# Performance work log

Hardware: AMD Instinct MI355X
Metric: run time of the kernel (lower is better)

The kernel has to match this reference:

```python
import jax, jax.numpy as jnp
import numpy as np

B, S, D, H = 4, 2048, 1024, 16
HD = D // H  # 64


def setup_inputs() -> dict:
    key = jax.random.key(0)
    ks = jax.random.split(key, 16)
    inv = 1.0 / np.sqrt(D)
    inv_hd = 1.0 / np.sqrt(D)
    inp = {
        "query": jax.random.normal(ks[0], (B, S, D), jnp.float32),
        "key": jax.random.normal(ks[1], (B, S, D), jnp.float32),
        "value": jax.random.normal(ks[2], (B, S, D), jnp.float32),
        # causal mask: True entries are masked out (masked_fill semantics)
        "mask": jnp.triu(jnp.ones((S, S), jnp.bool_), k=1),
        # weights stored [in, out] (math identical to torch x @ W.T)
        "Wq": jax.random.normal(ks[3], (D, D), jnp.float32) * inv,
        "Wk": jax.random.normal(ks[4], (D, D), jnp.float32) * inv,
        "Wv": jax.random.normal(ks[5], (D, D), jnp.float32) * inv,
        "wq_h": jax.random.normal(ks[6], (D, HD), jnp.float32) * inv_hd,
        "bq_h": jax.random.normal(ks[7], (HD,), jnp.float32) * inv_hd,
        "wk_h": jax.random.normal(ks[8], (D, HD), jnp.float32) * inv_hd,
        "bk_h": jax.random.normal(ks[9], (HD,), jnp.float32) * inv_hd,
        "wv_h": jax.random.normal(ks[10], (D, HD), jnp.float32) * inv_hd,
        "bv_h": jax.random.normal(ks[11], (HD,), jnp.float32) * inv_hd,
        "Wo": jax.random.normal(ks[12], (D, D), jnp.float32) * inv,
    }
    return inp


def reference(query, key, value, mask, Wq, Wk, Wv, wq_h, bq_h, wk_h, bk_h, wv_h, bv_h, Wo):
    # full-width projections
    q = jnp.einsum('bsd,de->bse', query, Wq)
    k = jnp.einsum('bsd,de->bse', key, Wk)
    v = jnp.einsum('bsd,de->bse', value, Wv)
    # per-head projections: the torch loop reuses the SAME weights every
    # iteration, so all H head outputs are identical -> compute once.
    qh = jnp.einsum('bsd,dh->bsh', q, wq_h) + bq_h  # [B,S,HD]
    kh = jnp.einsum('bsd,dh->bsh', k, wk_h) + bk_h
    vh = jnp.einsum('bsd,dh->bsh', v, wv_h) + bv_h
    scores = jnp.einsum('bsh,bth->bst', qh, kh) / jnp.sqrt(jnp.float32(HD))
    scores = jnp.where(mask, jnp.float32(-1e9), scores)
    attn = jax.nn.softmax(scores, axis=-1)
    out_h = jnp.einsum('bst,bth->bsh', attn, vh)  # [B,S,HD]
    out = jnp.tile(out_h, (1, 1, H))  # cat of H identical heads -> [B,S,D]
    # final linear; dropout is identity at inference
    return jnp.einsum('bsd,de->bse', out, Wo)
```

## Files before the change

### kernel.cpp

```cpp
#include <hip/hip_runtime.h>
#include <math.h>

#define S_LEN 2048
#define BATCH 4
#define DMODEL 1024
#define HDIM 64
#define NROWS (BATCH * S_LEN)

typedef __attribute__((ext_vector_type(8))) short bf16x8;
typedef __attribute__((ext_vector_type(4))) float f32x4;

__device__ inline ushort f2bf(float f) {
    union { float f; uint u; } v{f};
    uint r = v.u + 0x7fffu + ((v.u >> 16) & 1u);
    return (ushort)(r >> 16);
}

__device__ inline bf16x8 cvt8(float4 a, float4 b) {
    bf16x8 r;
    r[0] = (short)f2bf(a.x); r[1] = (short)f2bf(a.y);
    r[2] = (short)f2bf(a.z); r[3] = (short)f2bf(a.w);
    r[4] = (short)f2bf(b.x); r[5] = (short)f2bf(b.y);
    r[6] = (short)f2bf(b.z); r[7] = (short)f2bf(b.w);
    return r;
}

__global__ __launch_bounds__(256) void transpose_wh(
    const float* __restrict__ B0, const float* __restrict__ B1, const float* __restrict__ B2,
    ushort* __restrict__ T0, ushort* __restrict__ T1, ushort* __restrict__ T2)
{
    const int z = blockIdx.y;
    const float* B = (z == 0) ? B0 : (z == 1) ? B1 : B2;
    ushort* T      = (z == 0) ? T0 : (z == 1) ? T1 : T2;
    const int kr0 = blockIdx.x * 64;
    __shared__ ushort Ts[64][72];
    const int t = threadIdx.x;

    #pragma unroll
    for (int q = 0; q < 4; ++q) {
        int u   = t * 4 + q;
        int row = u >> 4;
        int c4  = (u & 15) << 2;
        float4 v = *reinterpret_cast<const float4*>(
            B + (size_t)(kr0 + row) * 64 + c4);
        Ts[row][c4 + 0] = f2bf(v.x); Ts[row][c4 + 1] = f2bf(v.y);
        Ts[row][c4 + 2] = f2bf(v.z); Ts[row][c4 + 3] = f2bf(v.w);
    }
    __syncthreads();
    #pragma unroll
    for (int q = 0; q < 2; ++q) {
        int u  = t * 2 + q;
        int h  = u >> 3;
        int k8 = (u & 7) << 3;
        uint4 o;
        uint* ow = reinterpret_cast<uint*>(&o);
        #pragma unroll
        for (int i = 0; i < 4; ++i)
            ow[i] = (uint)Ts[k8 + 2 * i][h] | ((uint)Ts[k8 + 2 * i + 1][h] << 16);
        *reinterpret_cast<uint4*>(T + (size_t)h * 1024 + kr0 + k8) = o;
    }
}

__global__ __launch_bounds__(256) void prep_direct(
    const float* __restrict__ A0, const float* __restrict__ A1, const float* __restrict__ A2,
    const ushort* __restrict__ W0, const ushort* __restrict__ W1, const ushort* __restrict__ W2,
    ushort* __restrict__ T0, ushort* __restrict__ T1, ushort* __restrict__ T2)
{
    const int z = blockIdx.y;
    const float* A  = (z == 0) ? A0 : (z == 1) ? A1 : A2;
    const ushort* W = (z == 0) ? W0 : (z == 1) ? W1 : W2;
    ushort* T       = (z == 0) ? T0 : (z == 1) ? T1 : T2;

    __shared__ float Pr[4][16][64];

    const int t    = threadIdx.x;
    const int w    = t >> 6;
    const int lane = t & 63;
    const int lg   = lane >> 4;
    const int lc   = lane & 15;
    const int r0   = blockIdx.x * 16;

    const float*  Ap = A + (size_t)(r0 + lc) * 1024 + (w << 8) + (lg << 3);
    const ushort* Bp = W + (size_t)lc * 1024 + (w << 8) + (lg << 3);

    f32x4 acc[4] = {};
    float4 a0[2], a1[2];
    uint4  bl[2][4];

    #pragma unroll
    for (int d = 0; d < 2; ++d) {
        a0[d] = *reinterpret_cast<const float4*>(Ap + d * 32);
        a1[d] = *reinterpret_cast<const float4*>(Ap + d * 32 + 4);
        #pragma unroll
        for (int n = 0; n < 4; ++n)
            bl[d][n] = *reinterpret_cast<const uint4*>(Bp + n * 16384 + d * 32);
    }

    #pragma unroll
    for (int ks = 0; ks < 8; ++ks) {
        const int d = ks & 1;
        bf16x8 af = cvt8(a0[d], a1[d]);
        bf16x8 bfr[4];
        #pragma unroll
        for (int n = 0; n < 4; ++n)
            bfr[n] = __builtin_bit_cast(bf16x8, bl[d][n]);
        if (ks < 6) {
            a0[d] = *reinterpret_cast<const float4*>(Ap + (ks + 2) * 32);
            a1[d] = *reinterpret_cast<const float4*>(Ap + (ks + 2) * 32 + 4);
            #pragma unroll
            for (int n = 0; n < 4; ++n)
                bl[d][n] = *reinterpret_cast<const uint4*>(Bp + n * 16384 + (ks + 2) * 32);
        }
        #pragma unroll
        for (int n = 0; n < 4; ++n)
            acc[n] = __builtin_amdgcn_mfma_f32_16x16x32_bf16(af, bfr[n], acc[n], 0, 0, 0);
    }

    #pragma unroll
    for (int n = 0; n < 4; ++n)
        #pragma unroll
        for (int reg = 0; reg < 4; ++reg)
            Pr[w][4 * lg + reg][16 * n + lc] = acc[n][reg];
    __syncthreads();

    const int row = t >> 4;
    const int col = (t & 15) << 2;
    float s[4];
    #pragma unroll
    for (int i = 0; i < 4; ++i)
        s[i] = Pr[0][row][col + i] + Pr[1][row][col + i] +
               Pr[2][row][col + i] + Pr[3][row][col + i];
    #pragma unroll
    for (int i = 0; i < 4; ++i)
        T[(size_t)(col + i) * 1024 + r0 + row] = f2bf(s[i]);
}

__global__ __launch_bounds__(64) void proj_sw(
    const float* __restrict__ A0, const float* __restrict__ A1, const float* __restrict__ A2,
    const ushort* __restrict__ W0, const ushort* __restrict__ W1, const ushort* __restrict__ W2,
    const float* __restrict__ b0, const float* __restrict__ b1, const float* __restrict__ b2,
    ushort* __restrict__ O0, ushort* __restrict__ O1, ushort* __restrict__ O2)
{
    const int z = blockIdx.y;
    const float* A    = (z == 0) ? A0 : (z == 1) ? A1 : A2;
    const ushort* W   = (z == 0) ? W0 : (z == 1) ? W1 : W2;
    const float* bias = (z == 0) ? b0 : (z == 1) ? b1 : b2;
    ushort* O         = (z == 0) ? O0 : (z == 1) ? O1 : O2;

    __shared__ __align__(16) ushort Abuf[2][16][64];

    const int l  = threadIdx.x;
    const int lg = l >> 4;
    const int lc = l & 15;
    const int wu = lc >> 1;
    const int wh = lc & 1;
    const int r0 = blockIdx.x * 16;

    f32x4 acc[4] = {};

#define LOADA(R, c)                                                           \
    _Pragma("unroll")                                                         \
    for (int j = 0; j < 4; ++j)                                               \
        R[j] = *reinterpret_cast<const float4*>(                              \
            A + (size_t)(r0 + 4 * j + lg) * 1024 + (c) * 64 + lc * 4);

#define PROCESS(c, R, BUF)                                                    \
    {                                                                         \
        bf16x8 bfr[4][2];                                                     \
        _Pragma("unroll")                                                     \
        for (int a = 0; a < 4; ++a)                                           \
            _Pragma("unroll")                                                 \
            for (int s = 0; s < 2; ++s)                                       \
                bfr[a][s] = *reinterpret_cast<const bf16x8*>(                 \
                    W + (size_t)(16 * a + lc) * 1024 + (c) * 64 + s * 32 +    \
                    lg * 8);                                                  \
        _Pragma("unroll")                                                     \
        for (int j = 0; j < 4; ++j) {                                         \
            uint2 pk;                                                         \
            pk.x = (uint)f2bf(R[j].x) | ((uint)f2bf(R[j].y) << 16);           \
            pk.y = (uint)f2bf(R[j].z) | ((uint)f2bf(R[j].w) << 16);           \
            int row = 4 * j + lg;                                             \
            char* dst = (char*)Abuf + (BUF) * 2048 + row * 128 +              \
                        ((wu ^ (row & 7)) << 4) + wh * 8;                     \
            *reinterpret_cast<uint2*>(dst) = pk;                              \
        }                                                                     \
        _Pragma("unroll")                                                     \
        for (int s = 0; s < 2; ++s) {                                         \
            const char* src = (const char*)Abuf + (BUF) * 2048 + lc * 128 +   \
                              (((s * 4 + lg) ^ (lc & 7)) << 4);               \
            bf16x8 af = *reinterpret_cast<const bf16x8*>(src);                \
            _Pragma("unroll")                                                 \
            for (int a = 0; a < 4; ++a)                                       \
                acc[a] = __builtin_amdgcn_mfma_f32_16x16x32_bf16(             \
                    af, bfr[a][s], acc[a], 0, 0, 0);                          \
        }                                                                     \
    }

    float4 ra[4], rb[4];
    LOADA(ra, 0)
    #pragma unroll
    for (int cc = 0; cc < 8; ++cc) {
        LOADA(rb, 2 * cc + 1)
        PROCESS(2 * cc, ra, 0)
        if (cc < 7) LOADA(ra, 2 * cc + 2)
        PROCESS(2 * cc + 1, rb, 1)
    }
#undef LOADA
#undef PROCESS

    #pragma unroll
    for (int a = 0; a < 4; ++a) {
        float bv = bias[16 * a + lc];
        #pragma unroll
        for (int reg = 0; reg < 4; ++reg)
            O[(size_t)(r0 + 4 * lg + reg) * 64 + 16 * a + lc] =
                f2bf(acc[a][reg] + bv);
    }
}

__global__ __launch_bounds__(256) void fold_wo(const float* __restrict__ Wo,
                                               ushort* __restrict__ WoT)
{
    int idx = blockIdx.x * 256 + threadIdx.x;
    int j = idx >> 10;
    int e = idx & 1023;
    float s = 0.f;
    #pragma unroll
    for (int h = 0; h < 16; ++h)
        s += Wo[(size_t)((h << 6) + j) * 1024 + e];
    WoT[(size_t)e * 64 + j] = f2bf(s);
}

__global__ __launch_bounds__(256) void transpose_v(const ushort* __restrict__ vh,
                                                   ushort* __restrict__ vhT)
{
    const int b  = blockIdx.y;
    const int r0 = blockIdx.x * 64;
    __shared__ ushort T[64][72];
    const int t = threadIdx.x;

    #pragma unroll
    for (int q = 0; q < 2; ++q) {
        int u  = t * 2 + q;
        int s  = u >> 3;
        int d8 = (u & 7) << 3;
        uint4 v = *reinterpret_cast<const uint4*>(
            vh + ((size_t)b * S_LEN + r0 + s) * 64 + d8);
        *reinterpret_cast<uint4*>(&T[s][d8]) = v;
    }
    __syncthreads();
    #pragma unroll
    for (int q = 0; q < 2; ++q) {
        int u  = t * 2 + q;
        int d  = u >> 3;
        int s8 = (u & 7) << 3;
        uint4 o;
        uint* ow = reinterpret_cast<uint*>(&o);
        #pragma unroll
        for (int i = 0; i < 4; ++i)
            ow[i] = (uint)T[s8 + 2 * i][d] | ((uint)T[s8 + 2 * i + 1][d] << 16);
        *reinterpret_cast<uint4*>(
            vhT + (size_t)b * 64 * S_LEN + (size_t)d * S_LEN + r0 + s8) = o;
    }
}

__global__ __launch_bounds__(256) void flash_mfma(
    const ushort* __restrict__ qh, const ushort* __restrict__ kh,
    const ushort* __restrict__ vhT,
    float* __restrict__ Opart, float* __restrict__ mpart, float* __restrict__ lpart)
{
    const int b = blockIdx.y;
    const int u = blockIdx.x;
    int gi = 0;
    #pragma unroll
    for (int gg = 0; gg < 7; ++gg)
        if (u >= 2 * (gg + 1) * (gg + 2)) gi = gg + 1;
    const int rem = u - 2 * gi * (gi + 1);
    const int dq  = rem / (gi + 1);
    const int c   = rem - dq * (gi + 1);
    const int qt  = 4 * gi + dq;
    const int r0  = qt * 64;
    const int kvbase = c << 8;
    const int slot = b * 144 + u;

    __shared__ ushort Qs[64][72];
    __shared__ ushort Ks[64][72];
    __shared__ ushort Vt[64][72];
    __shared__ ushort Pw[4][16][72];

    const int t    = threadIdx.x;
    const int w    = t >> 6;
    const int lane = t & 63;
    const int lg   = lane >> 4;
    const int lc   = lane & 15;

    const ushort* qb  = qh  + (size_t)b * S_LEN * 64;
    const ushort* kb  = kh  + (size_t)b * S_LEN * 64;
    const ushort* vtb = vhT + (size_t)b * 64 * S_LEN;

    #pragma unroll
    for (int q = 0; q < 2; ++q) {
        int uu  = t * 2 + q;
        int row = uu >> 3;
        int c8  = (uu & 7) << 3;
        *reinterpret_cast<uint4*>(&Qs[row][c8]) =
            *reinterpret_cast<const uint4*>(qb + (size_t)(r0 + row) * 64 + c8);
    }
    __syncthreads();
    bf16x8 qf0 = *reinterpret_cast<const bf16x8*>(&Qs[16 * w + lc][lg * 8]);
    bf16x8 qf1 = *reinterpret_cast<const bf16x8*>(&Qs[16 * w + lc][32 + lg * 8]);

    f32x4 od[4] = {};
    float m = -INFINITY, lsum = 0.f;
    const int qrow = r0 + 16 * w + lc;

    const int ntt = min(4, ((r0 + 63 - kvbase) >> 6) + 1);
    for (int tt = 0; tt < ntt; ++tt) {
        const int t0 = kvbase + (tt << 6);
        __syncthreads();
        #pragma unroll
        for (int q = 0; q < 2; ++q) {
            int uu  = t * 2 + q;
            int row = uu >> 3;
            int c8  = (uu & 7) << 3;
            *reinterpret_cast<uint4*>(&Ks[row][c8]) =
                *reinterpret_cast<const uint4*>(kb + (size_t)(t0 + row) * 64 + c8);
            *reinterpret_cast<uint4*>(&Vt[row][c8]) =
                *reinterpret_cast<const uint4*>(vtb + (size_t)row * S_LEN + t0 + c8);
        }
        __syncthreads();

        if (t0 <= r0 + 16 * w + 15) {
            f32x4 s[4] = {};
            #pragma unroll
            for (int a = 0; a < 4; ++a) {
                bf16x8 kf0 = *reinterpret_cast<const bf16x8*>(&Ks[16 * a + lc][lg * 8]);
                bf16x8 kf1 = *reinterpret_cast<const bf16x8*>(&Ks[16 * a + lc][32 + lg * 8]);
                s[a] = __builtin_amdgcn_mfma_f32_16x16x32_bf16(kf0, qf0, s[a], 0, 0, 0);
                s[a] = __builtin_amdgcn_mfma_f32_16x16x32_bf16(kf1, qf1, s[a], 0, 0, 0);
            }
            float rm = -1e30f;
            #pragma unroll
            for (int a = 0; a < 4; ++a)
                #pragma unroll
                for (int reg = 0; reg < 4; ++reg) {
                    int kv = t0 + 16 * a + 4 * lg + reg;
                    float v = s[a][reg] * 0.125f;
                    if (kv > qrow) v = -1e30f;
                    s[a][reg] = v;
                    rm = fmaxf(rm, v);
                }
            rm = fmaxf(rm, __shfl_xor(rm, 16));
            rm = fmaxf(rm, __shfl_xor(rm, 32));
            float mn = fmaxf(m, rm);
            float sc = __expf(m - mn);
            float rs = 0.f;
            #pragma unroll
            for (int a = 0; a < 4; ++a)
                #pragma unroll
                for (int reg = 0; reg < 4; ++reg) {
                    float p = __expf(s[a][reg] - mn);
                    s[a][reg] = p;
                    rs += p;
                }
            rs += __shfl_xor(rs, 16);
            rs += __shfl_xor(rs, 32);
            lsum = lsum * sc + rs;
            m = mn;
            #pragma unroll
            for (int di = 0; di < 4; ++di) od[di] *= sc;

            #pragma unroll
            for (int a = 0; a < 4; ++a)
                #pragma unroll
                for (int rp = 0; rp < 2; ++rp) {
                    uint pk = (uint)f2bf(s[a][2 * rp]) |
                              ((uint)f2bf(s[a][2 * rp + 1]) << 16);
                    *reinterpret_cast<uint*>(&Pw[w][lc][16 * a + 4 * lg + 2 * rp]) = pk;
                }
            bf16x8 pf0 = *reinterpret_cast<const bf16x8*>(&Pw[w][lc][lg * 8]);
            bf16x8 pf1 = *reinterpret_cast<const bf16x8*>(&Pw[w][lc][32 + lg * 8]);
            #pragma unroll
            for (int di = 0; di < 4; ++di) {
                bf16x8 vf0 = *reinterpret_cast<const bf16x8*>(&Vt[16 * di + lc][lg * 8]);
                bf16x8 vf1 = *reinterpret_cast<const bf16x8*>(&Vt[16 * di + lc][32 + lg * 8]);
                od[di] = __builtin_amdgcn_mfma_f32_16x16x32_bf16(vf0, pf0, od[di], 0, 0, 0);
                od[di] = __builtin_amdgcn_mfma_f32_16x16x32_bf16(vf1, pf1, od[di], 0, 0, 0);
            }
        }
    }

    #pragma unroll
    for (int di = 0; di < 4; ++di)
        #pragma unroll
        for (int reg = 0; reg < 4; ++reg)
            Opart[(size_t)slot * 4096 + (16 * di + 4 * lg + reg) * 64 + 16 * w + lc] =
                od[di][reg];
    if (lg == 0) {
        mpart[slot * 64 + 16 * w + lc] = m;
        lpart[slot * 64 + 16 * w + lc] = lsum;
    }
}

__global__ __launch_bounds__(256) void flash_combine(
    const float* __restrict__ Opart, const float* __restrict__ mpart,
    const float* __restrict__ lpart, ushort* __restrict__ oh)
{
    const int qt = blockIdx.x, b = blockIdx.y;
    const int gi = qt >> 2;
    const int nc = gi + 1;
    const int ubase = 2 * gi * (gi + 1) + (qt & 3) * (gi + 1);
    __shared__ float T[64][65];

    const int t  = threadIdx.x;
    const int q  = t & 63;
    const int d0 = (t >> 6) << 4;

    float mc[8];
    float M = -INFINITY;
    #pragma unroll
    for (int cc = 0; cc < 8; ++cc) {
        mc[cc] = (cc < nc) ? mpart[(b * 144 + ubase + cc) * 64 + q] : -INFINITY;
        M = fmaxf(M, mc[cc]);
    }
    float L = 0.f;
    float acc[16] = {};
    for (int cc = 0; cc < nc; ++cc) {
        const int slot = b * 144 + ubase + cc;
        float wgt = __expf(mc[cc] - M);
        L += lpart[slot * 64 + q] * wgt;
        const float* op = Opart + (size_t)slot * 4096 + q;
        #pragma unroll
        for (int i = 0; i < 16; ++i)
            acc[i] += wgt * op[(d0 + i) * 64];
    }
    float inv = 1.f / L;
    #pragma unroll
    for (int i = 0; i < 16; ++i) T[q][d0 + i] = acc[i] * inv;
    __syncthreads();

    const int q2 = t >> 2;
    const int ds = (t & 3) << 4;
    uint wbuf[8];
    #pragma unroll
    for (int i = 0; i < 8; ++i)
        wbuf[i] = (uint)f2bf(T[q2][ds + 2 * i]) |
                  ((uint)f2bf(T[q2][ds + 2 * i + 1]) << 16);
    ushort* dst = oh + ((size_t)b * S_LEN + qt * 64 + q2) * 64 + ds;
    uint4 o1, o2;
    o1.x = wbuf[0]; o1.y = wbuf[1]; o1.z = wbuf[2]; o1.w = wbuf[3];
    o2.x = wbuf[4]; o2.y = wbuf[5]; o2.z = wbuf[6]; o2.w = wbuf[7];
    *reinterpret_cast<uint4*>(dst)     = o1;
    *reinterpret_cast<uint4*>(dst + 8) = o2;
}

__global__ __launch_bounds__(256) void epilogue_mfma(
    const ushort* __restrict__ oh, const ushort* __restrict__ WoT,
    float* __restrict__ out)
{
    const int r0 = blockIdx.x * 64;
    const int c0 = blockIdx.y * 128;
    __shared__ ushort As[64][72];
    __shared__ ushort Bs[128][72];

    const int t    = threadIdx.x;
    const int w    = t >> 6;
    const int lane = t & 63;
    const int lg   = lane >> 4;
    const int lc   = lane & 15;

    #pragma unroll
    for (int q = 0; q < 2; ++q) {
        int u   = t * 2 + q;
        int row = u >> 3;
        int c8  = (u & 7) << 3;
        *reinterpret_cast<uint4*>(&As[row][c8]) =
            *reinterpret_cast<const uint4*>(oh + (size_t)(r0 + row) * 64 + c8);
    }
    #pragma unroll
    for (int q = 0; q < 4; ++q) {
        int u   = t * 4 + q;
        int row = u >> 3;
        int c8  = (u & 7) << 3;
        *reinterpret_cast<uint4*>(&Bs[row][c8]) =
            *reinterpret_cast<const uint4*>(WoT + (size_t)(c0 + row) * 64 + c8);
    }
    __syncthreads();

    bf16x8 af0 = *reinterpret_cast<const bf16x8*>(&As[16 * w + lc][lg * 8]);
    bf16x8 af1 = *reinterpret_cast<const bf16x8*>(&As[16 * w + lc][32 + lg * 8]);
    f32x4 acc[8] = {};
    #pragma unroll
    for (int n = 0; n < 8; ++n) {
        bf16x8 bf0 = *reinterpret_cast<const bf16x8*>(&Bs[16 * n + lc][lg * 8]);
        bf16x8 bf1 = *reinterpret_cast<const bf16x8*>(&Bs[16 * n + lc][32 + lg * 8]);
        acc[n] = __builtin_amdgcn_mfma_f32_16x16x32_bf16(af0, bf0, acc[n], 0, 0, 0);
        acc[n] = __builtin_amdgcn_mfma_f32_16x16x32_bf16(af1, bf1, acc[n], 0, 0, 0);
    }
    #pragma unroll
    for (int n = 0; n < 8; ++n)
        #pragma unroll
        for (int reg = 0; reg < 4; ++reg)
            out[(size_t)(r0 + 16 * w + 4 * lg + reg) * 1024 + c0 + 16 * n + lc] =
                acc[n][reg];
}

extern "C" void kernel_launch(void* const* d_in, const int* in_sizes, int n_in,
                              void* d_out, int out_size, void* d_ws, size_t ws_size,
                              hipStream_t stream)
{
    const float* query = (const float*)d_in[0];
    const float* key   = (const float*)d_in[1];
    const float* value = (const float*)d_in[2];
    const float* Wq   = (const float*)d_in[4];
    const float* Wk   = (const float*)d_in[5];
    const float* Wv   = (const float*)d_in[6];
    const float* wq_h = (const float*)d_in[7];
    const float* bq_h = (const float*)d_in[8];
    const float* wk_h = (const float*)d_in[9];
    const float* bk_h = (const float*)d_in[10];
    const float* wv_h = (const float*)d_in[11];
    const float* bv_h = (const float*)d_in[12];
    const float* Wo   = (const float*)d_in[13];
    float* out = (float*)d_out;

    ushort* W16  = (ushort*)d_ws;
    ushort* WT0  = W16;
    ushort* WT1  = W16 + 65536;
    ushort* WT2  = W16 + 131072;
    ushort* WoT  = W16 + 196608;
    ushort* qh   = W16 + 262144;
    ushort* kh   = qh + 524288;
    ushort* vh   = kh + 524288;
    ushort* vhT  = vh + 524288;
    ushort* oh   = vhT + 524288;
    ushort* whT0 = oh + 524288;
    ushort* whT1 = whT0 + 65536;
    ushort* whT2 = whT1 + 65536;

    float* Opart = out;
    float* mpart = out + 2359296;
    float* lpart = out + 2396160;

    transpose_wh<<<dim3(16, 3), 256, 0, stream>>>(
        wq_h, wk_h, wv_h, whT0, whT1, whT2);
    fold_wo<<<256, 256, 0, stream>>>(Wo, WoT);

    prep_direct<<<dim3(64, 3), 256, 0, stream>>>(
        Wq, Wk, Wv, whT0, whT1, whT2, WT0, WT1, WT2);

    proj_sw<<<dim3(512, 3), 64, 0, stream>>>(
        query, key, value, WT0, WT1, WT2, bq_h, bk_h, bv_h, qh, kh, vh);

    transpose_v<<<dim3(S_LEN / 64, BATCH), 256, 0, stream>>>(vh, vhT);

    flash_mfma<<<dim3(144, BATCH), 256, 0, stream>>>(
        qh, kh, vhT, Opart, mpart, lpart);
    flash_combine<<<dim3(S_LEN / 64, BATCH), 256, 0, stream>>>(
        Opart, mpart, lpart, oh);

    epilogue_mfma<<<dim3(NROWS / 64, DMODEL / 128), 256, 0, stream>>>(oh, WoT, out);
}
```

Baseline: 85.81 us.

## Split projection K dimension across four waves with LDS reduction

The folded projection kernel goes from one wave per 16-row block to four waves, each handling a quarter of the 1024-wide K dimension. Partial accumulators are reduced through shared memory, then bias is added and the result stored with vectorized writes. This gives each block more parallelism and shortens the serial K loop, addressing latency limits from too few waves in flight. The cost is more LDS use, a block-wide barrier and reduction traffic.

```diff
diff --git a/kernel.cpp b/kernel.cpp
--- a/kernel.cpp
+++ b/kernel.cpp
@@ -135,7 +135,7 @@
         T[(size_t)(col + i) * 1024 + r0 + row] = f2bf(s[i]);
 }
 
-__global__ __launch_bounds__(64) void proj_sw(
+__global__ __launch_bounds__(256) void proj_4w(
     const float* __restrict__ A0, const float* __restrict__ A1, const float* __restrict__ A2,
     const ushort* __restrict__ W0, const ushort* __restrict__ W1, const ushort* __restrict__ W2,
     const float* __restrict__ b0, const float* __restrict__ b1, const float* __restrict__ b2,
@@ -147,14 +147,18 @@
     const float* bias = (z == 0) ? b0 : (z == 1) ? b1 : b2;
     ushort* O         = (z == 0) ? O0 : (z == 1) ? O1 : O2;
 
-    __shared__ __align__(16) ushort Abuf[2][16][64];
-
-    const int l  = threadIdx.x;
+    __shared__ __align__(16) ushort Abuf[4][2][16][64];
+    __shared__ float Pr[4][16][64];
+
+    const int t  = threadIdx.x;
+    const int w  = t >> 6;
+    const int l  = t & 63;
     const int lg = l >> 4;
     const int lc = l & 15;
     const int wu = lc >> 1;
     const int wh = lc & 1;
     const int r0 = blockIdx.x * 16;
+    const int kb = w << 8;
 
     f32x4 acc[4] = {};
 
@@ -162,7 +166,7 @@
     _Pragma("unroll")                                                         \
     for (int j = 0; j < 4; ++j)                                               \
         R[j] = *reinterpret_cast<const float4*>(                              \
-            A + (size_t)(r0 + 4 * j + lg) * 1024 + (c) * 64 + lc * 4);
+            A + (size_t)(r0 + 4 * j + lg) * 1024 + kb + (c) * 64 + lc * 4);
 
 #define PROCESS(c, R, BUF)                                                    \
     {                                                                         \
@@ -172,21 +176,21 @@
             _Pragma("unroll")                                                 \
             for (int s = 0; s < 2; ++s)                                       \
                 bfr[a][s] = *reinterpret_cast<const bf16x8*>(                 \
-                    W + (size_t)(16 * a + lc) * 1024 + (c) * 64 + s * 32 +    \
-                    lg * 8);                                                  \
+                    W + (size_t)(16 * a + lc) * 1024 + kb + (c) * 64 +        \
+                    s * 32 + lg * 8);                                         \
         _Pragma("unroll")                                                     \
         for (int j = 0; j < 4; ++j) {                                         \
             uint2 pk;                                                         \
             pk.x = (uint)f2bf(R[j].x) | ((uint)f2bf(R[j].y) << 16);           \
             pk.y = (uint)f2bf(R[j].z) | ((uint)f2bf(R[j].w) << 16);           \
             int row = 4 * j + lg;                                             \
-            char* dst = (char*)Abuf + (BUF) * 2048 + row * 128 +              \
+            char* dst = (char*)&Abuf[w][BUF][0][0] + row * 128 +              \
                         ((wu ^ (row & 7)) << 4) + wh * 8;                     \
             *reinterpret_cast<uint2*>(dst) = pk;                              \
         }                                                                     \
         _Pragma("unroll")                                                     \
         for (int s = 0; s < 2; ++s) {                                         \
-            const char* src = (const char*)Abuf + (BUF) * 2048 + lc * 128 +   \
+            const char* src = (const char*)&Abuf[w][BUF][0][0] + lc * 128 +   \
                               (((s * 4 + lg) ^ (lc & 7)) << 4);               \
             bf16x8 af = *reinterpret_cast<const bf16x8*>(src);                \
             _Pragma("unroll")                                                 \
@@ -198,24 +202,33 @@
 
     float4 ra[4], rb[4];
     LOADA(ra, 0)
-    #pragma unroll
-    for (int cc = 0; cc < 8; ++cc) {
-        LOADA(rb, 2 * cc + 1)
-        PROCESS(2 * cc, ra, 0)
-        if (cc < 7) LOADA(ra, 2 * cc + 2)
-        PROCESS(2 * cc + 1, rb, 1)
-    }
+    LOADA(rb, 1)
+    PROCESS(0, ra, 0)
+    LOADA(ra, 2)
+    PROCESS(1, rb, 1)
+    LOADA(rb, 3)
+    PROCESS(2, ra, 0)
+    PROCESS(3, rb, 1)
 #undef LOADA
 #undef PROCESS
 
     #pragma unroll
-    for (int a = 0; a < 4; ++a) {
-        float bv = bias[16 * a + lc];
+    for (int a = 0; a < 4; ++a)
         #pragma unroll
         for (int reg = 0; reg < 4; ++reg)
-            O[(size_t)(r0 + 4 * lg + reg) * 64 + 16 * a + lc] =
-                f2bf(acc[a][reg] + bv);
-    }
+            Pr[w][4 * lg + reg][16 * a + lc] = acc[a][reg];
+    __syncthreads();
+
+    const int row = t >> 4;
+    const int col = (t & 15) << 2;
+    float4 bb = *reinterpret_cast<const float4*>(bias + col);
+    float s0 = Pr[0][row][col + 0] + Pr[1][row][col + 0] + Pr[2][row][col + 0] + Pr[3][row][col + 0] + bb.x;
+    float s1 = Pr[0][row][col + 1] + Pr[1][row][col + 1] + Pr[2][row][col + 1] + Pr[3][row][col + 1] + bb.y;
+    float s2 = Pr[0][row][col + 2] + Pr[1][row][col + 2] + Pr[2][row][col + 2] + Pr[3][row][col + 2] + bb.z;
+    float s3 = Pr[0][row][col + 3] + Pr[1][row][col + 3] + Pr[2][row][col + 3] + Pr[3][row][col + 3] + bb.w;
+    ushort4 o;
+    o.x = f2bf(s0); o.y = f2bf(s1); o.z = f2bf(s2); o.w = f2bf(s3);
+    *reinterpret_cast<ushort4*>(O + (size_t)(r0 + row) * 64 + col) = o;
 }
 
 __global__ __launch_bounds__(256) void fold_wo(const float* __restrict__ Wo,
@@ -549,7 +562,7 @@
     prep_direct<<<dim3(64, 3), 256, 0, stream>>>(
         Wq, Wk, Wv, whT0, whT1, whT2, WT0, WT1, WT2);
 
-    proj_sw<<<dim3(512, 3), 64, 0, stream>>>(
+    proj_4w<<<dim3(512, 3), 256, 0, stream>>>(
         query, key, value, WT0, WT1, WT2, bq_h, bk_h, bv_h, qh, kh, vh);
 
     transpose_v<<<dim3(S_LEN / 64, BATCH), 256, 0, stream>>>(vh, vhT);
```

Result: faster. 77.85 us (-9.3%).
